# Kernel optimization log

Measured on AMD Instinct MI355X. Metric: run time of the kernel, lower is better.

The kernel has to match this reference:

```python
import jax, jax.numpy as jnp
import numpy as np

B, C, N, K = 8, 256, 4096, 16

def setup_inputs() -> dict:
    key = jax.random.key(0)
    k1, k2, k3 = jax.random.split(key, 3)
    x = jax.random.normal(k1, (B, C, N, 1), dtype=jnp.float32)
    edge_index = jax.random.randint(k2, (2, B, N, K), 0, N, dtype=jnp.int64)
    eps = jnp.zeros((1,), dtype=jnp.float32)
    W = jax.random.normal(k3, (C, C), dtype=jnp.float32) * (1.0 / np.sqrt(C))
    b = jnp.zeros((C,), dtype=jnp.float32)
    return {"x": x, "edge_index": edge_index, "eps": eps, "W": W, "b": b}

def reference(x, edge_index, eps, W, b):
    # x: [B, C, N, 1]; edge_index: [2, B, N, K]
    idx = edge_index[0]                                  # [B, N, K] neighbor ids
    x_sq = x[..., 0]                                     # [B, C, N]
    # batched_index_select: gather neighbor features -> [B, C, N, K]
    gath = jnp.take_along_axis(
        x_sq, idx.reshape(B, 1, N * K).astype(jnp.int32), axis=2
    ).reshape(B, C, N, K)
    x_j = jnp.sum(gath, axis=-1, keepdims=True)          # [B, C, N, 1]
    h = (1.0 + eps[0]) * x + x_j                         # GIN update
    # BasicConv: 1x1 Conv2d + bias + ReLU
    out = jnp.einsum('oc,bcnk->bonk', W, h) + b[None, :, None, None]
    return jax.nn.relu(out)
```

## Files before the change

kernel.cpp:

```cpp
#include <hip/hip_runtime.h>
#include <stdint.h>

#define BB 8
#define CC 256
#define NN 4096
#define KK 16
#define NT 16

typedef float f32x4 __attribute__((ext_vector_type(4)));
typedef short bf16x8 __attribute__((ext_vector_type(8)));
typedef int   i32x4 __attribute__((ext_vector_type(4)));
typedef unsigned int u32x2 __attribute__((ext_vector_type(2)));
typedef unsigned int u32x4 __attribute__((ext_vector_type(4)));

__device__ __forceinline__ ushort f2bf(float f) {
  union { float f; uint32_t u; } v; v.f = f;
  uint32_t r = v.u + 0x7FFFu + ((v.u >> 16) & 1u);
  return (ushort)(r >> 16);
}
__device__ __forceinline__ float asf(uint32_t u) {
  union { uint32_t u; float f; } v; v.u = u; return v.f;
}

__global__ __launch_bounds__(256) void k_prep(
    const float* __restrict__ x, const float* __restrict__ W,
    ushort* __restrict__ xT, ushort* __restrict__ Wfrag)
{
  const int bid = blockIdx.x;
  const int t   = threadIdx.x;
  if (bid >= 2048) {
    const int wb = bid - 2048;
    const int o  = wb * 4 + (t >> 6);
    const int k0 = (t & 63) * 4;
    f32x4 v = __builtin_nontemporal_load((const f32x4*)(W + (size_t)o * CC + k0));
    ushort4 h;
    h.x = f2bf(v.x); h.y = f2bf(v.y); h.z = f2bf(v.z); h.w = f2bf(v.w);
    const int kc = k0 >> 5, ks = k0 & 31;
    *(ushort4*)(Wfrag + ((size_t)(kc * CC + o)) * 32 + ks) = h;
    return;
  }
  __shared__ float tile[64][68];
  const int b    = bid & 7;
  const int tl   = bid >> 3;
  const int c0   = (tl & 3) * 64;
  const int n0   = (tl >> 2) * 64;
  {
    const int r  = t >> 2;
    const int cs = (t & 3) * 16;
    const float* xp = x + ((size_t)b * CC + c0 + r) * NN + n0 + cs;
    #pragma unroll
    for (int i = 0; i < 4; ++i) {
      f32x4 v = __builtin_nontemporal_load((const f32x4*)(xp + i * 4));
      *(f32x4*)&tile[r][cs + i * 4] = v;
    }
  }
  __syncthreads();
  const int nl = t >> 2;
  const int cl = (t & 3) * 16;
  union { ushort s[16]; uint4 q[2]; } pk;
  #pragma unroll
  for (int i = 0; i < 16; ++i) pk.s[i] = f2bf(tile[cl + i][nl]);
  uint4* dst = (uint4*)(xT + ((size_t)b * NN + n0 + nl) * CC + c0 + cl);
  dst[0] = pk.q[0];
  dst[1] = pk.q[1];
}

__global__ __launch_bounds__(256) void k_fused(
    const ushort* __restrict__ xT, const int* __restrict__ edge0,
    const float* __restrict__ eps, const ushort* __restrict__ Wfrag,
    const float* __restrict__ bias, float* __restrict__ out)
{
  __shared__ ushort hLds[NT][264];
  const int bid = blockIdx.x;
  const int b   = bid & 7;
  const int n0  = (bid >> 3) * NT;
  const int t    = threadIdx.x;
  const int wave = t >> 6, lane = t & 63;
  const float epsv = 1.0f + eps[0];
  const ushort* xb = xT + (size_t)b * NN * CC;
  const int c4 = lane * 4;

  #pragma unroll
  for (int i = 0; i < NT / 4; ++i) {
    const int nl = wave * (NT / 4) + i;
    const int n  = n0 + nl;
    const i32x4* epv = (const i32x4*)(edge0 + ((size_t)b * NN + n) * KK);
    i32x4 e0 = __builtin_nontemporal_load(epv + 0);
    i32x4 e1 = __builtin_nontemporal_load(epv + 1);
    i32x4 e2 = __builtin_nontemporal_load(epv + 2);
    i32x4 e3 = __builtin_nontemporal_load(epv + 3);
    u32x2 sv = *(const u32x2*)(xb + (n << 8) + c4);

    const int js[16] = {e0.x, e0.y, e0.z, e0.w, e1.x, e1.y, e1.z, e1.w,
                        e2.x, e2.y, e2.z, e2.w, e3.x, e3.y, e3.z, e3.w};
    f32x4 acc = (f32x4){0.f, 0.f, 0.f, 0.f};
    #pragma unroll
    for (int k = 0; k < KK; ++k) {
      const int jr = __builtin_amdgcn_readfirstlane(js[k]);
      const ushort* rp = xb + ((size_t)jr << 8);
      u32x2 g = *(const u32x2*)(rp + c4);
      acc += (f32x4){asf(g.x << 16), asf(g.x & 0xffff0000u),
                     asf(g.y << 16), asf(g.y & 0xffff0000u)};
    }
    acc += (f32x4){asf(sv.x << 16), asf(sv.x & 0xffff0000u),
                   asf(sv.y << 16), asf(sv.y & 0xffff0000u)} * epsv;

    uint2 pk;
    pk.x = (uint32_t)f2bf(acc[0]) | ((uint32_t)f2bf(acc[1]) << 16);
    pk.y = (uint32_t)f2bf(acc[2]) | ((uint32_t)f2bf(acc[3]) << 16);
    *(uint2*)&hLds[nl][c4] = pk;
  }
  __syncthreads();

  f32x4 acc2[4];
  #pragma unroll
  for (int m = 0; m < 4; ++m) acc2[m] = (f32x4){0.f, 0.f, 0.f, 0.f};

  const int lrow = lane & 15;
  const int kgrp = lane >> 4;
  const int o0   = wave * 64;

  #pragma unroll
  for (int kc = 0; kc < 8; ++kc) {
    const int cs = kgrp * 8;
    bf16x8 bfr = *(const bf16x8*)&hLds[lrow][kc * 32 + cs];
    bf16x8 afr[4];
    #pragma unroll
    for (int m = 0; m < 4; ++m) {
      const uint32_t aoff = (uint32_t)(kc * CC + o0 + m * 16 + lrow) * 32 + cs;
      afr[m] = *(const bf16x8*)(Wfrag + aoff);
    }
    #pragma unroll
    for (int m = 0; m < 4; ++m)
      acc2[m] = __builtin_amdgcn_mfma_f32_16x16x32_bf16(
          afr[m], bfr, acc2[m], 0, 0, 0);
  }

  const int n = n0 + lrow;
  #pragma unroll
  for (int m = 0; m < 4; ++m) {
    const f32x4 bv4 = *(const f32x4*)(bias + o0 + m * 16 + kgrp * 4);
    #pragma unroll
    for (int r = 0; r < 4; ++r) {
      const int o = o0 + m * 16 + kgrp * 4 + r;
      float v = acc2[m][r] + bv4[r];
      v = v > 0.f ? v : 0.f;
      __builtin_nontemporal_store(v, &out[((size_t)b * CC + o) * NN + n]);
    }
  }
}

extern "C" void kernel_launch(void* const* d_in, const int* in_sizes, int n_in,
                              void* d_out, int out_size, void* d_ws, size_t ws_size,
                              hipStream_t stream) {
  const float* x    = (const float*)d_in[0];
  const int*   edge = (const int*)d_in[1];
  const float* eps  = (const float*)d_in[2];
  const float* W    = (const float*)d_in[3];
  const float* bias = (const float*)d_in[4];
  float* out = (float*)d_out;

  ushort* xT    = (ushort*)d_ws;
  ushort* Wfrag = xT + (size_t)BB * NN * CC;

  k_prep<<<2048 + 64, 256, 0, stream>>>(x, W, xT, Wfrag);

  k_fused<<<BB * (NN / NT), 256, 0, stream>>>(xT, edge, eps, Wfrag, bias, out);
}
```

Before: 143.7 us.

## Split fused gather+GEMM into separate kernels with larger GEMM N-tile

The fused gather+1x1-conv kernel becomes two kernels. The first writes the GIN aggregate h as a bf16 [B,N,C] buffer to global workspace. The second runs the GEMM with 64-node tiles, so each W fragment load feeds 4x more MFMAs and the output stores cover 64 contiguous nodes instead of 16. The cost is a global round trip for h (about 16 MB written and read) plus an extra kernel launch, and the output stores are no longer nontemporal.

```diff
diff --git a/kernel.cpp b/kernel.cpp
--- a/kernel.cpp
+++ b/kernel.cpp
@@ -5,13 +5,11 @@
 #define CC 256
 #define NN 4096
 #define KK 16
-#define NT 16
 
 typedef float f32x4 __attribute__((ext_vector_type(4)));
 typedef short bf16x8 __attribute__((ext_vector_type(8)));
 typedef int   i32x4 __attribute__((ext_vector_type(4)));
 typedef unsigned int u32x2 __attribute__((ext_vector_type(2)));
-typedef unsigned int u32x4 __attribute__((ext_vector_type(4)));
 
 __device__ __forceinline__ ushort f2bf(float f) {
   union { float f; uint32_t u; } v; v.f = f;
@@ -65,25 +63,22 @@
   dst[1] = pk.q[1];
 }
 
-__global__ __launch_bounds__(256) void k_fused(
+__global__ __launch_bounds__(256) void k_gather(
     const ushort* __restrict__ xT, const int* __restrict__ edge0,
-    const float* __restrict__ eps, const ushort* __restrict__ Wfrag,
-    const float* __restrict__ bias, float* __restrict__ out)
+    const float* __restrict__ eps, ushort* __restrict__ hT)
 {
-  __shared__ ushort hLds[NT][264];
   const int bid = blockIdx.x;
   const int b   = bid & 7;
-  const int n0  = (bid >> 3) * NT;
-  const int t    = threadIdx.x;
-  const int wave = t >> 6, lane = t & 63;
+  const int n0  = (bid >> 3) * 16;
+  const int wave = threadIdx.x >> 6, lane = threadIdx.x & 63;
   const float epsv = 1.0f + eps[0];
   const ushort* xb = xT + (size_t)b * NN * CC;
+  ushort*       hb = hT + (size_t)b * NN * CC;
   const int c4 = lane * 4;
 
   #pragma unroll
-  for (int i = 0; i < NT / 4; ++i) {
-    const int nl = wave * (NT / 4) + i;
-    const int n  = n0 + nl;
+  for (int i = 0; i < 4; ++i) {
+    const int n = n0 + wave * 4 + i;
     const i32x4* epv = (const i32x4*)(edge0 + ((size_t)b * NN + n) * KK);
     i32x4 e0 = __builtin_nontemporal_load(epv + 0);
     i32x4 e1 = __builtin_nontemporal_load(epv + 1);
@@ -108,13 +103,36 @@
     uint2 pk;
     pk.x = (uint32_t)f2bf(acc[0]) | ((uint32_t)f2bf(acc[1]) << 16);
     pk.y = (uint32_t)f2bf(acc[2]) | ((uint32_t)f2bf(acc[3]) << 16);
-    *(uint2*)&hLds[nl][c4] = pk;
+    *(uint2*)(hb + (n << 8) + c4) = pk;
+  }
+}
+
+__global__ __launch_bounds__(256) void k_gemm(
+    const ushort* __restrict__ hT, const ushort* __restrict__ Wfrag,
+    const float* __restrict__ bias, float* __restrict__ out)
+{
+  __shared__ ushort hLds[64][264];
+  const int bid = blockIdx.x;
+  const int b   = bid & 7;
+  const int n0  = (bid >> 3) * 64;
+  const int t    = threadIdx.x;
+  const int wave = t >> 6, lane = t & 63;
+
+  {
+    const int row  = t >> 2;
+    const int coff = (t & 3) * 64;
+    const ushort* src = hT + (size_t)b * NN * CC + ((size_t)(n0 + row) << 8) + coff;
+    #pragma unroll
+    for (int i = 0; i < 8; ++i)
+      *(uint4*)&hLds[row][coff + i * 8] = *(const uint4*)(src + i * 8);
   }
   __syncthreads();
 
-  f32x4 acc2[4];
+  f32x4 acc[4][4];
   #pragma unroll
-  for (int m = 0; m < 4; ++m) acc2[m] = (f32x4){0.f, 0.f, 0.f, 0.f};
+  for (int m = 0; m < 4; ++m)
+    #pragma unroll
+    for (int nn = 0; nn < 4; ++nn) acc[m][nn] = (f32x4){0.f, 0.f, 0.f, 0.f};
 
   const int lrow = lane & 15;
   const int kgrp = lane >> 4;
@@ -123,29 +141,36 @@
   #pragma unroll
   for (int kc = 0; kc < 8; ++kc) {
     const int cs = kgrp * 8;
-    bf16x8 bfr = *(const bf16x8*)&hLds[lrow][kc * 32 + cs];
-    bf16x8 afr[4];
+    bf16x8 afr[4], bfr[4];
     #pragma unroll
     for (int m = 0; m < 4; ++m) {
       const uint32_t aoff = (uint32_t)(kc * CC + o0 + m * 16 + lrow) * 32 + cs;
       afr[m] = *(const bf16x8*)(Wfrag + aoff);
     }
     #pragma unroll
+    for (int nn = 0; nn < 4; ++nn)
+      bfr[nn] = *(const bf16x8*)&hLds[nn * 16 + lrow][kc * 32 + cs];
+    #pragma unroll
     for (int m = 0; m < 4; ++m)
-      acc2[m] = __builtin_amdgcn_mfma_f32_16x16x32_bf16(
-          afr[m], bfr, acc2[m], 0, 0, 0);
+      #pragma unroll
+      for (int nn = 0; nn < 4; ++nn)
+        acc[m][nn] = __builtin_amdgcn_mfma_f32_16x16x32_bf16(
+            afr[m], bfr[nn], acc[m][nn], 0, 0, 0);
   }
 
-  const int n = n0 + lrow;
   #pragma unroll
   for (int m = 0; m < 4; ++m) {
     const f32x4 bv4 = *(const f32x4*)(bias + o0 + m * 16 + kgrp * 4);
     #pragma unroll
     for (int r = 0; r < 4; ++r) {
       const int o = o0 + m * 16 + kgrp * 4 + r;
-      float v = acc2[m][r] + bv4[r];
-      v = v > 0.f ? v : 0.f;
-      __builtin_nontemporal_store(v, &out[((size_t)b * CC + o) * NN + n]);
+      #pragma unroll
+      for (int nn = 0; nn < 4; ++nn) {
+        const int n = n0 + nn * 16 + lrow;
+        float v = acc[m][nn][r] + bv4[r];
+        v = v > 0.f ? v : 0.f;
+        out[((size_t)b * CC + o) * NN + n] = v;
+      }
     }
   }
 }
@@ -161,9 +186,12 @@
   float* out = (float*)d_out;
 
   ushort* xT    = (ushort*)d_ws;
-  ushort* Wfrag = xT + (size_t)BB * NN * CC;
+  ushort* hT    = xT + (size_t)BB * NN * CC;
+  ushort* Wfrag = hT + (size_t)BB * NN * CC;
 
   k_prep<<<2048 + 64, 256, 0, stream>>>(x, W, xT, Wfrag);
 
-  k_fused<<<BB * (NN / NT), 256, 0, stream>>>(xT, edge, eps, Wfrag, bias, out);
+  k_gather<<<BB * (NN / 16), 256, 0, stream>>>(xT, edge, eps, hT);
+
+  k_gemm<<<BB * (NN / 64), 256, 0, stream>>>(hT, Wfrag, bias, out);
 }
```

Result: faster. 138.0 us (-4.0%).

## Apply 1x1 conv before neighbor gather using linearity, then gather projected features

Applied to the files above, without the earlier changes.

Uses linearity to compute y = W·x first (a GEMM fused with the transpose and bf16 conversion) and then gathers and sums neighbor rows of y, adding bias and ReLU in the gather kernel. The GEMM now runs directly in the prep stage with a 32-node tile, and the gather kernel writes its output through an LDS transpose so global stores are coalesced float4 rather than scattered scalars. This adds a third launch and a separate W-prep kernel, and it changes the rounding order (bf16 rounding of W·x before summation).

```diff
diff --git a/kernel.cpp b/kernel.cpp
--- a/kernel.cpp
+++ b/kernel.cpp
@@ -5,13 +5,11 @@
 #define CC 256
 #define NN 4096
 #define KK 16
-#define NT 16
 
 typedef float f32x4 __attribute__((ext_vector_type(4)));
 typedef short bf16x8 __attribute__((ext_vector_type(8)));
 typedef int   i32x4 __attribute__((ext_vector_type(4)));
 typedef unsigned int u32x2 __attribute__((ext_vector_type(2)));
-typedef unsigned int u32x4 __attribute__((ext_vector_type(4)));
 
 __device__ __forceinline__ ushort f2bf(float f) {
   union { float f; uint32_t u; } v; v.f = f;
@@ -21,75 +19,126 @@
 __device__ __forceinline__ float asf(uint32_t u) {
   union { uint32_t u; float f; } v; v.u = u; return v.f;
 }
+__device__ __forceinline__ float bf2f(ushort h) {
+  union { uint32_t u; float f; } v; v.u = ((uint32_t)h) << 16;
+  return v.f;
+}
 
-__global__ __launch_bounds__(256) void k_prep(
-    const float* __restrict__ x, const float* __restrict__ W,
-    ushort* __restrict__ xT, ushort* __restrict__ Wfrag)
+__global__ __launch_bounds__(256) void k_wprep(
+    const float* __restrict__ W, ushort* __restrict__ Wfrag)
 {
+  const int t  = threadIdx.x;
+  const int o  = blockIdx.x * 4 + (t >> 6);
+  const int k0 = (t & 63) * 4;
+  f32x4 v = __builtin_nontemporal_load((const f32x4*)(W + (size_t)o * CC + k0));
+  ushort4 h;
+  h.x = f2bf(v.x); h.y = f2bf(v.y); h.z = f2bf(v.z); h.w = f2bf(v.w);
+  const int kc = k0 >> 5, ks = k0 & 31;
+  *(ushort4*)(Wfrag + ((size_t)(kc * CC + o)) * 32 + ks) = h;
+}
+
+__global__ __launch_bounds__(256) void k_conv(
+    const float* __restrict__ x, const ushort* __restrict__ Wfrag,
+    ushort* __restrict__ yT)
+{
+  __shared__ float  ftile[64][36];
+  __shared__ ushort xlds[32][264];
   const int bid = blockIdx.x;
-  const int t   = threadIdx.x;
-  if (bid >= 2048) {
-    const int wb = bid - 2048;
-    const int o  = wb * 4 + (t >> 6);
-    const int k0 = (t & 63) * 4;
-    f32x4 v = __builtin_nontemporal_load((const f32x4*)(W + (size_t)o * CC + k0));
-    ushort4 h;
-    h.x = f2bf(v.x); h.y = f2bf(v.y); h.z = f2bf(v.z); h.w = f2bf(v.w);
-    const int kc = k0 >> 5, ks = k0 & 31;
-    *(ushort4*)(Wfrag + ((size_t)(kc * CC + o)) * 32 + ks) = h;
-    return;
+  const int b   = bid & 7;
+  const int n0  = (bid >> 3) * 32;
+  const int t    = threadIdx.x;
+  const int wave = t >> 6, lane = t & 63;
+
+  const int r  = t >> 2;
+  const int cs = (t & 3) * 4;
+  const int nl = t >> 3;
+  const int cl = (t & 7) * 8;
+  #pragma unroll
+  for (int cb = 0; cb < 4; ++cb) {
+    const float* xp = x + ((size_t)(b * CC + cb * 64 + r)) * NN + n0 + cs;
+    f32x4 v0 = __builtin_nontemporal_load((const f32x4*)xp);
+    f32x4 v1 = __builtin_nontemporal_load((const f32x4*)(xp + 16));
+    __syncthreads();
+    *(f32x4*)&ftile[r][cs]      = v0;
+    *(f32x4*)&ftile[r][cs + 16] = v1;
+    __syncthreads();
+    union { ushort s[8]; uint4 q; } pk;
+    #pragma unroll
+    for (int i = 0; i < 8; ++i) pk.s[i] = f2bf(ftile[cl + i][nl]);
+    *(uint4*)&xlds[nl][cb * 64 + cl] = pk.q;
   }
-  __shared__ float tile[64][68];
-  const int b    = bid & 7;
-  const int tl   = bid >> 3;
-  const int c0   = (tl & 3) * 64;
-  const int n0   = (tl >> 2) * 64;
-  {
-    const int r  = t >> 2;
-    const int cs = (t & 3) * 16;
-    const float* xp = x + ((size_t)b * CC + c0 + r) * NN + n0 + cs;
+  __syncthreads();
+
+  f32x4 acc[4][2];
+  #pragma unroll
+  for (int m = 0; m < 4; ++m)
     #pragma unroll
-    for (int i = 0; i < 4; ++i) {
-      f32x4 v = __builtin_nontemporal_load((const f32x4*)(xp + i * 4));
-      *(f32x4*)&tile[r][cs + i * 4] = v;
+    for (int nn = 0; nn < 2; ++nn) acc[m][nn] = (f32x4){0.f, 0.f, 0.f, 0.f};
+
+  const int lrow = lane & 15;
+  const int kgrp = lane >> 4;
+  const int o0   = wave * 64;
+
+  #pragma unroll
+  for (int kc = 0; kc < 8; ++kc) {
+    const int c2 = kgrp * 8;
+    bf16x8 afr[4], bfr[2];
+    #pragma unroll
+    for (int m = 0; m < 4; ++m) {
+      const uint32_t aoff = (uint32_t)(kc * CC + o0 + m * 16 + lrow) * 32 + c2;
+      afr[m] = *(const bf16x8*)(Wfrag + aoff);
+    }
+    #pragma unroll
+    for (int nn = 0; nn < 2; ++nn)
+      bfr[nn] = *(const bf16x8*)&xlds[nn * 16 + lrow][kc * 32 + c2];
+    #pragma unroll
+    for (int m = 0; m < 4; ++m)
+      #pragma unroll
+      for (int nn = 0; nn < 2; ++nn)
+        acc[m][nn] = __builtin_amdgcn_mfma_f32_16x16x32_bf16(
+            afr[m], bfr[nn], acc[m][nn], 0, 0, 0);
+  }
+
+  #pragma unroll
+  for (int m = 0; m < 4; ++m) {
+    #pragma unroll
+    for (int nn = 0; nn < 2; ++nn) {
+      const int n = n0 + nn * 16 + lrow;
+      const int o = o0 + m * 16 + kgrp * 4;
+      uint2 pk2;
+      pk2.x = (uint32_t)f2bf(acc[m][nn][0]) | ((uint32_t)f2bf(acc[m][nn][1]) << 16);
+      pk2.y = (uint32_t)f2bf(acc[m][nn][2]) | ((uint32_t)f2bf(acc[m][nn][3]) << 16);
+      *(uint2*)(yT + (((size_t)b * NN + n) << 8) + o) = pk2;
     }
   }
-  __syncthreads();
-  const int nl = t >> 2;
-  const int cl = (t & 3) * 16;
-  union { ushort s[16]; uint4 q[2]; } pk;
-  #pragma unroll
-  for (int i = 0; i < 16; ++i) pk.s[i] = f2bf(tile[cl + i][nl]);
-  uint4* dst = (uint4*)(xT + ((size_t)b * NN + n0 + nl) * CC + c0 + cl);
-  dst[0] = pk.q[0];
-  dst[1] = pk.q[1];
 }
 
-__global__ __launch_bounds__(256) void k_fused(
-    const ushort* __restrict__ xT, const int* __restrict__ edge0,
-    const float* __restrict__ eps, const ushort* __restrict__ Wfrag,
-    const float* __restrict__ bias, float* __restrict__ out)
+__global__ __launch_bounds__(256) void k_gout(
+    const ushort* __restrict__ yT, const int* __restrict__ edge0,
+    const float* __restrict__ eps, const float* __restrict__ bias,
+    float* __restrict__ out)
 {
-  __shared__ ushort hLds[NT][264];
+  __shared__ float res[32][264];
   const int bid = blockIdx.x;
   const int b   = bid & 7;
-  const int n0  = (bid >> 3) * NT;
+  const int n0  = (bid >> 3) * 32;
   const int t    = threadIdx.x;
   const int wave = t >> 6, lane = t & 63;
   const float epsv = 1.0f + eps[0];
-  const ushort* xb = xT + (size_t)b * NN * CC;
+  const ushort* yb = yT + (size_t)b * NN * CC;
   const int c4 = lane * 4;
+  const f32x4 bv = *(const f32x4*)(bias + c4);
 
   #pragma unroll
-  for (int i = 0; i < NT / 4; ++i) {
-    const int nl = wave * (NT / 4) + i;
+  for (int i = 0; i < 8; ++i) {
+    const int nl = wave * 8 + i;
     const int n  = n0 + nl;
     const i32x4* epv = (const i32x4*)(edge0 + ((size_t)b * NN + n) * KK);
     i32x4 e0 = __builtin_nontemporal_load(epv + 0);
     i32x4 e1 = __builtin_nontemporal_load(epv + 1);
     i32x4 e2 = __builtin_nontemporal_load(epv + 2);
     i32x4 e3 = __builtin_nontemporal_load(epv + 3);
-    u32x2 sv = *(const u32x2*)(xb + (n << 8) + c4);
+    u32x2 sv = *(const u32x2*)(yb + ((size_t)n << 8) + c4);
 
     const int js[16] = {e0.x, e0.y, e0.z, e0.w, e1.x, e1.y, e1.z, e1.w,
                         e2.x, e2.y, e2.z, e2.w, e3.x, e3.y, e3.z, e3.w};
@@ -97,56 +146,27 @@
     #pragma unroll
     for (int k = 0; k < KK; ++k) {
       const int jr = __builtin_amdgcn_readfirstlane(js[k]);
-      const ushort* rp = xb + ((size_t)jr << 8);
+      const ushort* rp = yb + ((size_t)jr << 8);
       u32x2 g = *(const u32x2*)(rp + c4);
       acc += (f32x4){asf(g.x << 16), asf(g.x & 0xffff0000u),
                      asf(g.y << 16), asf(g.y & 0xffff0000u)};
     }
     acc += (f32x4){asf(sv.x << 16), asf(sv.x & 0xffff0000u),
                    asf(sv.y << 16), asf(sv.y & 0xffff0000u)} * epsv;
-
-    uint2 pk;
-    pk.x = (uint32_t)f2bf(acc[0]) | ((uint32_t)f2bf(acc[1]) << 16);
-    pk.y = (uint32_t)f2bf(acc[2]) | ((uint32_t)f2bf(acc[3]) << 16);
-    *(uint2*)&hLds[nl][c4] = pk;
+    acc += bv;
+    #pragma unroll
+    for (int j = 0; j < 4; ++j) acc[j] = acc[j] > 0.f ? acc[j] : 0.f;
+    *(f32x4*)&res[nl][c4] = acc;
   }
   __syncthreads();
 
-  f32x4 acc2[4];
+  float* op = out + ((size_t)b * CC + t) * NN + n0;
   #pragma unroll
-  for (int m = 0; m < 4; ++m) acc2[m] = (f32x4){0.f, 0.f, 0.f, 0.f};
-
-  const int lrow = lane & 15;
-  const int kgrp = lane >> 4;
-  const int o0   = wave * 64;
-
-  #pragma unroll
-  for (int kc = 0; kc < 8; ++kc) {
-    const int cs = kgrp * 8;
-    bf16x8 bfr = *(const bf16x8*)&hLds[lrow][kc * 32 + cs];
-    bf16x8 afr[4];
+  for (int ch = 0; ch < 8; ++ch) {
+    f32x4 v;
     #pragma unroll
-    for (int m = 0; m < 4; ++m) {
-      const uint32_t aoff = (uint32_t)(kc * CC + o0 + m * 16 + lrow) * 32 + cs;
-      afr[m] = *(const bf16x8*)(Wfrag + aoff);
-    }
-    #pragma unroll
-    for (int m = 0; m < 4; ++m)
-      acc2[m] = __builtin_amdgcn_mfma_f32_16x16x32_bf16(
-          afr[m], bfr, acc2[m], 0, 0, 0);
-  }
-
-  const int n = n0 + lrow;
-  #pragma unroll
-  for (int m = 0; m < 4; ++m) {
-    const f32x4 bv4 = *(const f32x4*)(bias + o0 + m * 16 + kgrp * 4);
-    #pragma unroll
-    for (int r = 0; r < 4; ++r) {
-      const int o = o0 + m * 16 + kgrp * 4 + r;
-      float v = acc2[m][r] + bv4[r];
-      v = v > 0.f ? v : 0.f;
-      __builtin_nontemporal_store(v, &out[((size_t)b * CC + o) * NN + n]);
-    }
+    for (int j = 0; j < 4; ++j) v[j] = res[ch * 4 + j][t];
+    *(f32x4*)(op + ch * 4) = v;
   }
 }
 
@@ -160,10 +180,12 @@
   const float* bias = (const float*)d_in[4];
   float* out = (float*)d_out;
 
-  ushort* xT    = (ushort*)d_ws;
-  ushort* Wfrag = xT + (size_t)BB * NN * CC;
+  ushort* yT    = (ushort*)d_ws;
+  ushort* Wfrag = yT + (size_t)BB * NN * CC;
 
-  k_prep<<<2048 + 64, 256, 0, stream>>>(x, W, xT, Wfrag);
+  k_wprep<<<CC / 4, 256, 0, stream>>>(W, Wfrag);
 
-  k_fused<<<BB * (NN / NT), 256, 0, stream>>>(xT, edge, eps, Wfrag, bias, out);
+  k_conv<<<BB * (NN / 32), 256, 0, stream>>>(x, Wfrag, yT);
+
+  k_gout<<<BB * (NN / 32), 256, 0, stream>>>(yT, edge, eps, bias, out);
 }
```

After: 141.2 us. No clear change (-1.8%).
